# Performance work log

Hardware: AMD Instinct MI355X
Metric: run time of the kernel (lower is better)

The kernel has to match this reference:

```python
import jax, jax.numpy as jnp
import numpy as np

BIG = 3.4028234e+38  # torch fill value used as additive mask
EPS = 1e-5           # nn.LayerNorm default eps


def _layernorm(x):
    mu = jnp.mean(x, axis=-1, keepdims=True)
    var = jnp.mean(jnp.square(x - mu), axis=-1, keepdims=True)
    return (x - mu) / jnp.sqrt(var + EPS)


def setup_inputs() -> dict:
    key = jax.random.key(0)
    ks = jax.random.split(key, 12)
    B, N, H, S = 32, 512, 256, 3  # batch, num_codes, embedding_size, num_stacks
    features = jax.random.normal(ks[0], (B, N, H), dtype=jnp.float32)
    masks = jnp.ones((B, N, 1), dtype=jnp.float32)
    guide = jax.random.randint(ks[1], (B, N, N), 0, 2).astype(jnp.float32)
    prior_guide = jax.random.uniform(ks[2], (B, N, N), dtype=jnp.float32)
    sc = 0.02
    WQ = jax.random.normal(ks[3], (S, H, H), dtype=jnp.float32) * sc
    WK = jax.random.normal(ks[4], (S, H, H), dtype=jnp.float32) * sc
    WV = jax.random.normal(ks[5], (S, H, H), dtype=jnp.float32) * sc
    W1 = jax.random.normal(ks[6], (S, H, H), dtype=jnp.float32) * sc
    b1 = jnp.zeros((S, H), dtype=jnp.float32)
    W2 = jax.random.normal(ks[7], (S, H, H), dtype=jnp.float32) * sc
    b2 = jnp.zeros((S, H), dtype=jnp.float32)
    return {"features": features, "masks": masks, "guide": guide,
            "prior_guide": prior_guide, "WQ": WQ, "WK": WK, "WV": WV,
            "W1": W1, "b1": b1, "W2": W2, "b2": b2}


def reference(features, masks, guide, prior_guide, WQ, WK, WV, W1, b1, W2, b2):
    H = features.shape[-1]
    scale = 1.0 / jnp.sqrt(jnp.float32(H))
    attention_mask = jnp.where(masks[:, :, 0] != 0, 0.0, BIG)  # [B,N]
    inf_mask = jnp.where(guide != 0, 0.0, BIG)                 # [B,N,N]
    attentions = []
    x = features
    for i in range(WQ.shape[0]):
        f = masks * x                                          # [B,N,H]
        if i == 0:
            att = prior_guide[:, None, :, :]                   # use_prior path
        else:
            q = jnp.einsum('bnh,hd->bnd', f, WQ[i].T)          # nn.Linear: x @ W^T
            k = jnp.einsum('bnh,hd->bnd', f, WK[i].T)
            pre = jnp.einsum('bqd,bkd->bqk', q, k) * scale     # [B,N,N] (heads=1)
            pre = pre - attention_mask[:, None, :] - inf_mask
            att = jax.nn.softmax(pre, axis=-1)[:, None, :, :]  # [B,1,N,N]
        attentions.append(att)
        v = jnp.einsum('bnh,hd->bnd', f, WV[i].T)              # [B,N,H]
        post = jnp.einsum('bqk,bkh->bqh', att[:, 0], v)        # squeeze head dim
        post = _layernorm(post + f)
        ffn = jnp.maximum(jnp.einsum('bnh,hd->bnd', post, W1[i].T) + b1[i], 0.0)
        ffn = jnp.einsum('bnh,hd->bnd', ffn, W2[i].T) + b2[i]
        x = _layernorm(ffn + post)
    return x * masks, jnp.stack(attentions)
```

## Files before the change

kernel.cpp:

```cpp
#include <hip/hip_runtime.h>
#include <cstdint>
#include <cstddef>

#define B_ 32
#define N_ 512
#define H_ 256
#define S_ 3
#define BN_ (B_*N_)
#define HH_ (H_*H_)
#define BIGF 3.4028234e+38f
#define EPSF 1e-5f

typedef __bf16 bf16x8 __attribute__((ext_vector_type(8)));
typedef float  f32x4  __attribute__((ext_vector_type(4)));

typedef const void __attribute__((address_space(1)))* gas_t;
typedef void __attribute__((address_space(3)))* las_t;

__device__ __forceinline__ void async16(const unsigned short* g, unsigned short* l) {
  __builtin_amdgcn_global_load_lds((gas_t)g, (las_t)l, 16, 0, 0);
}

__device__ __forceinline__ unsigned short f2bf(float f) {
  __bf16 h = (__bf16)f;
  unsigned short s;
  __builtin_memcpy(&s, &h, 2);
  return s;
}
__device__ __forceinline__ float bf2f(unsigned short u) {
  unsigned int v = ((unsigned int)u) << 16;
  float f;
  __builtin_memcpy(&f, &v, 4);
  return f;
}

#define KC_STAGE(lane) ((((lane) & 3) ^ (((lane) >> 3) & 3)) * 8)
#define KC_READ(quad, l15) ((((quad) ^ (((l15) >> 1) & 3))) * 8)

__global__ __launch_bounds__(256) void cvt_all_k(
    const float* __restrict__ WQ, const float* __restrict__ WK,
    const float* __restrict__ WV, const float* __restrict__ W1,
    const float* __restrict__ W2,
    unsigned short* __restrict__ wqk, unsigned short* __restrict__ wv,
    unsigned short* __restrict__ w1, unsigned short* __restrict__ w2) {
  const int per = S_ * HH_ / 4;
  int gi = blockIdx.x * 256 + threadIdx.x;
  int which = gi / per;
  int e4 = gi - which * per;
  float4 v;
  if      (which == 0) v = ((const float4*)WQ)[e4];
  else if (which == 1) v = ((const float4*)WK)[e4];
  else if (which == 2) v = ((const float4*)WV)[e4];
  else if (which == 3) v = ((const float4*)W1)[e4];
  else                 v = ((const float4*)W2)[e4];
  ushort4 o;
  o.x = f2bf(v.x); o.y = f2bf(v.y); o.z = f2bf(v.z); o.w = f2bf(v.w);
  int e = e4 * 4;
  if (which <= 1) {
    int L = e / HH_, off = e - L * HH_;
    *(ushort4*)&wqk[(size_t)L * 2 * HH_ + (which == 1 ? HH_ : 0) + off] = o;
  } else if (which == 2) ((ushort4*)wv)[e4] = o;
  else if   (which == 3) ((ushort4*)w1)[e4] = o;
  else                   ((ushort4*)w2)[e4] = o;
}

__global__ __launch_bounds__(256) void mask_mul_k(
    const float* __restrict__ x, const float* __restrict__ masks,
    unsigned short* __restrict__ fb) {
  int i = blockIdx.x * 256 + threadIdx.x;
  int row = i >> 6;
  float m = masks[row];
  float4 v = ((const float4*)x)[i];
  ushort4 o;
  o.x = f2bf(v.x * m); o.y = f2bf(v.y * m); o.z = f2bf(v.z * m); o.w = f2bf(v.w * m);
  ((ushort4*)fb)[i] = o;
}

__global__ __launch_bounds__(256) void mfma_gemm_k(
    const unsigned short* __restrict__ A, const unsigned short* __restrict__ Bm,
    unsigned short* __restrict__ Cb,
    int K, int Nn, int lda, int ldb, long sA, long sB, long sC) {
  __shared__ __align__(16) unsigned short As[2][128 * 32];
  __shared__ __align__(16) unsigned short Bs[2][128 * 32];
  const int b = blockIdx.z;
  const int t = threadIdx.x;
  const int wave = t >> 6, lane = t & 63;
  const int wm = wave >> 1, wn = wave & 1;
  const int quad = lane >> 4, l15 = lane & 15;
  const int m0 = blockIdx.y * 128, n0 = blockIdx.x * 128;
  const int srow = lane >> 2;
  const int kc = KC_STAGE(lane);
  const int pos8 = (lane & 3) * 8;

  const unsigned short* pa0 = A + (size_t)b * sA + (size_t)(m0 + wave * 32 + srow) * lda + kc;
  const unsigned short* pa1 = pa0 + 16 * (size_t)lda;
  const unsigned short* pb0 = Bm + (size_t)b * sB + (size_t)(n0 + wave * 32 + srow) * ldb + kc;
  const unsigned short* pb1 = pb0 + 16 * (size_t)ldb;
  const int lo = (wave * 32 + srow) * 32 + pos8;

  f32x4 acc[4][4];
#pragma unroll
  for (int i = 0; i < 4; ++i)
#pragma unroll
    for (int j = 0; j < 4; ++j) acc[i][j] = (f32x4){0.f, 0.f, 0.f, 0.f};

  const int soff = KC_READ(quad, l15);
  const int NT = K >> 5;
  async16(pa0, &As[0][lo]); async16(pa1, &As[0][lo + 16 * 32]);
  async16(pb0, &Bs[0][lo]); async16(pb1, &Bs[0][lo + 16 * 32]);
  __syncthreads();
  int cur = 0;
  for (int tt = 0; tt < NT; ++tt) {
    if (tt + 1 < NT) {
      const int kn = (tt + 1) << 5;
      async16(pa0 + kn, &As[cur ^ 1][lo]); async16(pa1 + kn, &As[cur ^ 1][lo + 16 * 32]);
      async16(pb0 + kn, &Bs[cur ^ 1][lo]); async16(pb1 + kn, &Bs[cur ^ 1][lo + 16 * 32]);
    }
    bf16x8 af[4], bfr[4];
#pragma unroll
    for (int i = 0; i < 4; ++i)
      af[i] = *(const bf16x8*)&As[cur][(wm * 64 + i * 16 + l15) * 32 + soff];
#pragma unroll
    for (int j = 0; j < 4; ++j)
      bfr[j] = *(const bf16x8*)&Bs[cur][(wn * 64 + j * 16 + l15) * 32 + soff];
#pragma unroll
    for (int i = 0; i < 4; ++i)
#pragma unroll
      for (int j = 0; j < 4; ++j)
        acc[i][j] = __builtin_amdgcn_mfma_f32_16x16x32_bf16(af[i], bfr[j], acc[i][j], 0, 0, 0);
    __syncthreads();
    cur ^= 1;
  }

#pragma unroll
  for (int i = 0; i < 4; ++i) {
    const int rbase = m0 + wm * 64 + i * 16 + quad * 4;
#pragma unroll
    for (int j = 0; j < 4; ++j) {
      const int c = n0 + wn * 64 + j * 16 + l15;
#pragma unroll
      for (int r = 0; r < 4; ++r)
        Cb[(size_t)b * sC + (size_t)(rbase + r) * Nn + c] = f2bf(acc[i][j][r]);
    }
  }
}

template<int PRIOR>
__global__ __launch_bounds__(512) void ls_pv_k(
    const unsigned short* __restrict__ qk, const float* __restrict__ prior,
    const float* __restrict__ masks, const float* __restrict__ guide,
    const unsigned short* __restrict__ vT, const unsigned short* __restrict__ resb,
    float* __restrict__ att, float* __restrict__ post, unsigned short* __restrict__ postb) {
  __shared__ __align__(16) unsigned short As[2][64 * 32];
  __shared__ __align__(16) unsigned short Bs[2][512 * 32];
  __shared__ __align__(16) unsigned short Ps[64 * 520];
  __shared__ float red[4][64][2];
  const int b = blockIdx.x;
  const int t = threadIdx.x;
  const int wave = t >> 6, lane = t & 63;
  const int quad = lane >> 4, l15 = lane & 15;
  const int m0 = blockIdx.y * 64;
  const int srow = lane >> 2;
  const int kc = KC_STAGE(lane);
  const int pos8 = (lane & 3) * 8;
  const int soff = KC_READ(quad, l15);

  const unsigned short* vb = vT + (size_t)b * H_ * N_;
  const unsigned short* pv0 = vb + (size_t)(wave * 16 + srow) * N_ + kc;
  const unsigned short* pv1 = pv0 + (size_t)128 * N_;
  const int lvo = (wave * 16 + srow) * 32 + pos8;

  if (PRIOR) {
    async16(pv0, &Bs[0][lvo]);
    async16(pv1, &Bs[0][lvo + 128 * 32]);
    const float* src = prior + ((size_t)b * N_ + m0) * N_;
    float*       dst = att   + ((size_t)b * N_ + m0) * N_;
#pragma unroll
    for (int s = 0; s < 16; ++s) {
      int idx4 = s * 512 + t;
      float4 v = ((const float4*)src)[idx4];
      ((float4*)dst)[idx4] = v;
      int row = idx4 >> 7, col4 = idx4 & 127;
      ushort4 o;
      o.x = f2bf(v.x); o.y = f2bf(v.y); o.z = f2bf(v.z); o.w = f2bf(v.w);
      *(ushort4*)&Ps[row * 520 + col4 * 4] = o;
    }
    __syncthreads();
  } else {
    const int wm = wave >> 2, wn = wave & 3;
    const int ld = 2 * H_;
    const unsigned short* base = qk + (size_t)b * N_ * ld;
    const unsigned short* pa = base + (size_t)(m0 + wave * 16 + srow) * ld + kc;
    const unsigned short* pb = base + H_ + (size_t)(wave * 64 + srow) * ld + kc;
    const int lao = (wave * 16 + srow) * 32 + pos8;
    const int lbo = (wave * 64 + srow) * 32 + pos8;

    f32x4 acc[2][8];
#pragma unroll
    for (int i = 0; i < 2; ++i)
#pragma unroll
      for (int j = 0; j < 8; ++j) acc[i][j] = (f32x4){0.f, 0.f, 0.f, 0.f};

    if (wave < 4) async16(pa, &As[0][lao]);
#pragma unroll
    for (int c = 0; c < 4; ++c)
      async16(pb + (size_t)c * 16 * ld, &Bs[0][lbo + c * 16 * 32]);
    __syncthreads();
    int cur = 0;
#pragma unroll
    for (int tt = 0; tt < 8; ++tt) {
      if (tt < 7) {
        const int kn = (tt + 1) * 32;
        if (wave < 4) async16(pa + kn, &As[cur ^ 1][lao]);
#pragma unroll
        for (int c = 0; c < 4; ++c)
          async16(pb + (size_t)c * 16 * ld + kn, &Bs[cur ^ 1][lbo + c * 16 * 32]);
      }
      bf16x8 af[2], bfr[8];
#pragma unroll
      for (int i = 0; i < 2; ++i)
        af[i] = *(const bf16x8*)&As[cur][(wm * 32 + i * 16 + l15) * 32 + soff];
#pragma unroll
      for (int j = 0; j < 8; ++j)
        bfr[j] = *(const bf16x8*)&Bs[cur][(wn * 128 + j * 16 + l15) * 32 + soff];
#pragma unroll
      for (int i = 0; i < 2; ++i)
#pragma unroll
        for (int j = 0; j < 8; ++j)
          acc[i][j] = __builtin_amdgcn_mfma_f32_16x16x32_bf16(af[i], bfr[j], acc[i][j], 0, 0, 0);
      __syncthreads();
      cur ^= 1;
    }

    async16(pv0, &Bs[0][lvo]);
    async16(pv1, &Bs[0][lvo + 128 * 32]);

    float am[8];
#pragma unroll
    for (int j = 0; j < 8; ++j) {
      float mv = masks[(size_t)b * N_ + wn * 128 + j * 16 + l15];
      am[j] = (mv != 0.f) ? 0.f : BIGF;
    }
#pragma unroll
    for (int i = 0; i < 2; ++i) {
#pragma unroll
      for (int r = 0; r < 4; ++r) {
        const int mloc = wm * 32 + i * 16 + quad * 4 + r;
        const float* gr = guide + ((size_t)b * N_ + m0 + mloc) * N_;
        float mx = -BIGF;
#pragma unroll
        for (int j = 0; j < 8; ++j) {
          const int c = wn * 128 + j * 16 + l15;
          float g = gr[c];
          float v = acc[i][j][r] * 0.0625f - am[j] - ((g != 0.f) ? 0.f : BIGF);
          acc[i][j][r] = v;
          mx = fmaxf(mx, v);
        }
#pragma unroll
        for (int off = 1; off < 16; off <<= 1) mx = fmaxf(mx, __shfl_xor(mx, off));
        if (l15 == 0) red[wn][mloc][0] = mx;
      }
    }
    __syncthreads();
#pragma unroll
    for (int i = 0; i < 2; ++i) {
#pragma unroll
      for (int r = 0; r < 4; ++r) {
        const int mloc = wm * 32 + i * 16 + quad * 4 + r;
        float M = fmaxf(fmaxf(red[0][mloc][0], red[1][mloc][0]),
                        fmaxf(red[2][mloc][0], red[3][mloc][0]));
        float s = 0.f;
#pragma unroll
        for (int j = 0; j < 8; ++j) {
          float e = __expf(acc[i][j][r] - M);
          acc[i][j][r] = e;
          s += e;
        }
#pragma unroll
        for (int off = 1; off < 16; off <<= 1) s += __shfl_xor(s, off);
        if (l15 == 0) red[wn][mloc][1] = s;
      }
    }
    __syncthreads();
#pragma unroll
    for (int i = 0; i < 2; ++i) {
#pragma unroll
      for (int r = 0; r < 4; ++r) {
        const int mloc = wm * 32 + i * 16 + quad * 4 + r;
        float S = red[0][mloc][1] + red[1][mloc][1] + red[2][mloc][1] + red[3][mloc][1];
        float inv = 1.f / S;
        const size_t rowoff = ((size_t)b * N_ + m0 + mloc) * N_;
#pragma unroll
        for (int j = 0; j < 8; ++j) {
          const int c = wn * 128 + j * 16 + l15;
          float o = acc[i][j][r] * inv;
          att[rowoff + c] = o;
          Ps[mloc * 520 + c] = f2bf(o);
        }
      }
    }
    __syncthreads();
  }

  const int wm2 = wave >> 2, wn2 = wave & 3;

  f32x4 acc2[2][4];
#pragma unroll
  for (int i = 0; i < 2; ++i)
#pragma unroll
    for (int j = 0; j < 4; ++j) acc2[i][j] = (f32x4){0.f, 0.f, 0.f, 0.f};

  int cur = 0;
#pragma unroll
  for (int tt = 0; tt < 16; ++tt) {
    if (tt < 15) {
      const int kn = (tt + 1) * 32;
      async16(pv0 + kn, &Bs[cur ^ 1][lvo]);
      async16(pv1 + kn, &Bs[cur ^ 1][lvo + 128 * 32]);
    }
    bf16x8 af[2], bfr[4];
#pragma unroll
    for (int i = 0; i < 2; ++i)
      af[i] = *(const bf16x8*)&Ps[(wm2 * 32 + i * 16 + l15) * 520 + tt * 32 + quad * 8];
#pragma unroll
    for (int j = 0; j < 4; ++j)
      bfr[j] = *(const bf16x8*)&Bs[cur][(wn2 * 64 + j * 16 + l15) * 32 + soff];
#pragma unroll
    for (int i = 0; i < 2; ++i)
#pragma unroll
      for (int j = 0; j < 4; ++j)
        acc2[i][j] = __builtin_amdgcn_mfma_f32_16x16x32_bf16(af[i], bfr[j], acc2[i][j], 0, 0, 0);
    __syncthreads();
    cur ^= 1;
  }

#pragma unroll
  for (int i = 0; i < 2; ++i) {
#pragma unroll
    for (int r = 0; r < 4; ++r) {
      const int mloc = wm2 * 32 + i * 16 + quad * 4 + r;
      const long grow = (long)b * N_ + m0 + mloc;
      float s = 0.f, q = 0.f;
#pragma unroll
      for (int j = 0; j < 4; ++j) {
        const int c = wn2 * 64 + j * 16 + l15;
        float v = acc2[i][j][r] + bf2f(resb[grow * H_ + c]);
        acc2[i][j][r] = v;
        s += v; q += v * v;
      }
#pragma unroll
      for (int off = 1; off < 16; off <<= 1) {
        s += __shfl_xor(s, off);
        q += __shfl_xor(q, off);
      }
      if (l15 == 0) { red[wn2][mloc][0] = s; red[wn2][mloc][1] = q; }
    }
  }
  __syncthreads();
#pragma unroll
  for (int i = 0; i < 2; ++i) {
#pragma unroll
    for (int r = 0; r < 4; ++r) {
      const int mloc = wm2 * 32 + i * 16 + quad * 4 + r;
      const long grow = (long)b * N_ + m0 + mloc;
      float S = red[0][mloc][0] + red[1][mloc][0] + red[2][mloc][0] + red[3][mloc][0];
      float Q = red[0][mloc][1] + red[1][mloc][1] + red[2][mloc][1] + red[3][mloc][1];
      float mu = S * (1.f / H_);
      float var = Q * (1.f / H_) - mu * mu;
      float inv = 1.f / sqrtf(var + EPSF);
#pragma unroll
      for (int j = 0; j < 4; ++j) {
        const int c = wn2 * 64 + j * 16 + l15;
        float o = (acc2[i][j][r] - mu) * inv;
        post[grow * H_ + c] = o;
        postb[grow * H_ + c] = f2bf(o);
      }
    }
  }
}

template<int LAST>
__global__ __launch_bounds__(512) void ffn_k(
    const unsigned short* __restrict__ postb, const float* __restrict__ postf,
    const unsigned short* __restrict__ w1, const float* __restrict__ b1,
    const unsigned short* __restrict__ w2, const float* __restrict__ b2,
    const float* __restrict__ masks,
    unsigned short* __restrict__ fb, float* __restrict__ outx) {
  __shared__ __align__(16) unsigned short As[2][64 * 32];
  __shared__ __align__(16) unsigned short Bs[2][256 * 32];
  __shared__ __align__(16) unsigned short T1[64 * 264];
  __shared__ float red[4][64][2];
  const int t = threadIdx.x;
  const int wave = t >> 6, lane = t & 63;
  const int wm = wave >> 2, wn = wave & 3;
  const int quad = lane >> 4, l15 = lane & 15;
  const int m0 = blockIdx.y * 64;
  const int srow = lane >> 2;
  const int kc = KC_STAGE(lane);
  const int pos8 = (lane & 3) * 8;
  const int soff = KC_READ(quad, l15);

  const unsigned short* pa = postb + (size_t)(m0 + wave * 16 + srow) * H_ + kc;
  const int lao = (wave * 16 + srow) * 32 + pos8;
  const int lbo = (wave * 16 + srow) * 32 + pos8;

  const unsigned short* qb0 = w2 + (size_t)(wave * 16 + srow) * H_ + kc;
  const unsigned short* qb1 = qb0 + (size_t)128 * H_;

  {
    const unsigned short* pb0 = w1 + (size_t)(wave * 16 + srow) * H_ + kc;
    const unsigned short* pb1 = pb0 + (size_t)128 * H_;
    f32x4 acc[2][4];
#pragma unroll
    for (int i = 0; i < 2; ++i)
#pragma unroll
      for (int j = 0; j < 4; ++j) acc[i][j] = (f32x4){0.f, 0.f, 0.f, 0.f};
    if (wave < 4) async16(pa, &As[0][lao]);
    async16(pb0, &Bs[0][lbo]);
    async16(pb1, &Bs[0][lbo + 128 * 32]);
    __syncthreads();
    int cur = 0;
#pragma unroll
    for (int tt = 0; tt < 8; ++tt) {
      if (tt < 7) {
        const int kn = (tt + 1) * 32;
        if (wave < 4) async16(pa + kn, &As[cur ^ 1][lao]);
        async16(pb0 + kn, &Bs[cur ^ 1][lbo]);
        async16(pb1 + kn, &Bs[cur ^ 1][lbo + 128 * 32]);
      }
      bf16x8 af[2], bfr[4];
#pragma unroll
      for (int i = 0; i < 2; ++i)
        af[i] = *(const bf16x8*)&As[cur][(wm * 32 + i * 16 + l15) * 32 + soff];
#pragma unroll
      for (int j = 0; j < 4; ++j)
        bfr[j] = *(const bf16x8*)&Bs[cur][(wn * 64 + j * 16 + l15) * 32 + soff];
#pragma unroll
      for (int i = 0; i < 2; ++i)
#pragma unroll
        for (int j = 0; j < 4; ++j)
          acc[i][j] = __builtin_amdgcn_mfma_f32_16x16x32_bf16(af[i], bfr[j], acc[i][j], 0, 0, 0);
      __syncthreads();
      cur ^= 1;
    }

    async16(qb0, &Bs[0][lbo]);
    async16(qb1, &Bs[0][lbo + 128 * 32]);

    float bv[4];
#pragma unroll
    for (int j = 0; j < 4; ++j) bv[j] = b1[wn * 64 + j * 16 + l15];
#pragma unroll
    for (int i = 0; i < 2; ++i) {
#pragma unroll
      for (int r = 0; r < 4; ++r) {
        const int mloc = wm * 32 + i * 16 + quad * 4 + r;
#pragma unroll
        for (int j = 0; j < 4; ++j) {
          const int c = wn * 64 + j * 16 + l15;
          T1[mloc * 264 + c] = f2bf(fmaxf(acc[i][j][r] + bv[j], 0.f));
        }
      }
    }
  }
  __syncthreads();

  {
    f32x4 acc[2][4];
#pragma unroll
    for (int i = 0; i < 2; ++i)
#pragma unroll
      for (int j = 0; j < 4; ++j) acc[i][j] = (f32x4){0.f, 0.f, 0.f, 0.f};
    int cur = 0;
#pragma unroll
    for (int tt = 0; tt < 8; ++tt) {
      if (tt < 7) {
        const int kn = (tt + 1) * 32;
        async16(qb0 + kn, &Bs[cur ^ 1][lbo]);
        async16(qb1 + kn, &Bs[cur ^ 1][lbo + 128 * 32]);
      }
      bf16x8 af[2], bfr[4];
#pragma unroll
      for (int i = 0; i < 2; ++i)
        af[i] = *(const bf16x8*)&T1[(wm * 32 + i * 16 + l15) * 264 + tt * 32 + quad * 8];
#pragma unroll
      for (int j = 0; j < 4; ++j)
        bfr[j] = *(const bf16x8*)&Bs[cur][(wn * 64 + j * 16 + l15) * 32 + soff];
#pragma unroll
      for (int i = 0; i < 2; ++i)
#pragma unroll
        for (int j = 0; j < 4; ++j)
          acc[i][j] = __builtin_amdgcn_mfma_f32_16x16x32_bf16(af[i], bfr[j], acc[i][j], 0, 0, 0);
      __syncthreads();
      cur ^= 1;
    }
    float bv[4];
#pragma unroll
    for (int j = 0; j < 4; ++j) bv[j] = b2[wn * 64 + j * 16 + l15];
#pragma unroll
    for (int i = 0; i < 2; ++i) {
#pragma unroll
      for (int r = 0; r < 4; ++r) {
        const int mloc = wm * 32 + i * 16 + quad * 4 + r;
        const long grow = (long)m0 + mloc;
        float s = 0.f, q = 0.f;
#pragma unroll
        for (int j = 0; j < 4; ++j) {
          const int c = wn * 64 + j * 16 + l15;
          float v = acc[i][j][r] + bv[j] + postf[grow * H_ + c];
          acc[i][j][r] = v;
          s += v; q += v * v;
        }
#pragma unroll
        for (int off = 1; off < 16; off <<= 1) {
          s += __shfl_xor(s, off);
          q += __shfl_xor(q, off);
        }
        if (l15 == 0) { red[wn][mloc][0] = s; red[wn][mloc][1] = q; }
      }
    }
    __syncthreads();
#pragma unroll
    for (int i = 0; i < 2; ++i) {
#pragma unroll
      for (int r = 0; r < 4; ++r) {
        const int mloc = wm * 32 + i * 16 + quad * 4 + r;
        const long grow = (long)m0 + mloc;
        float S = red[0][mloc][0] + red[1][mloc][0] + red[2][mloc][0] + red[3][mloc][0];
        float Q = red[0][mloc][1] + red[1][mloc][1] + red[2][mloc][1] + red[3][mloc][1];
        float mu = S * (1.f / H_);
        float var = Q * (1.f / H_) - mu * mu;
        float inv = 1.f / sqrtf(var + EPSF);
        float mval = masks[grow];
#pragma unroll
        for (int j = 0; j < 4; ++j) {
          const int c = wn * 64 + j * 16 + l15;
          float o = (acc[i][j][r] - mu) * inv * mval;
          if (LAST) outx[grow * H_ + c] = o;
          else      fb[grow * H_ + c] = f2bf(o);
        }
      }
    }
  }
}

extern "C" void kernel_launch(void* const* d_in, const int* in_sizes, int n_in,
                              void* d_out, int out_size, void* d_ws, size_t ws_size,
                              hipStream_t stream) {
  const float* features = (const float*)d_in[0];
  const float* masks    = (const float*)d_in[1];
  const float* guide    = (const float*)d_in[2];
  const float* prior    = (const float*)d_in[3];
  const float* WQ       = (const float*)d_in[4];
  const float* WK       = (const float*)d_in[5];
  const float* WV       = (const float*)d_in[6];
  const float* W1       = (const float*)d_in[7];
  const float* b1       = (const float*)d_in[8];
  const float* W2       = (const float*)d_in[9];
  const float* b2       = (const float*)d_in[10];

  float* out     = (float*)d_out;
  float* out_x   = out;
  float* out_att = out + (size_t)BN_ * H_;

  char* w = (char*)d_ws;
  float* post = (float*)w;                     w += (size_t)BN_ * H_ * 4;
  unsigned short* f_bf   = (unsigned short*)w; w += (size_t)BN_ * H_ * 2;
  unsigned short* qk_bf  = (unsigned short*)w; w += (size_t)BN_ * 2 * H_ * 2;
  unsigned short* post_bf= (unsigned short*)w; w += (size_t)BN_ * H_ * 2;
  unsigned short* vT     = (unsigned short*)w; w += (size_t)BN_ * H_ * 2;
  unsigned short* wqk_bf = (unsigned short*)w; w += (size_t)S_ * 2 * HH_ * 2;
  unsigned short* wv_bf  = (unsigned short*)w; w += (size_t)S_ * HH_ * 2;
  unsigned short* w1_bf  = (unsigned short*)w; w += (size_t)S_ * HH_ * 2;
  unsigned short* w2_bf  = (unsigned short*)w; w += (size_t)S_ * HH_ * 2;

  dim3 g_cvt(5 * S_ * HH_ / 1024);
  dim3 g_ew(BN_ * H_ / 1024);
  dim3 g_qkp(4, BN_ / 128, 1);
  dim3 g_vt(4, 2, B_);
  dim3 g_ls(B_, N_ / 64, 1);
  dim3 g_ffn(1, BN_ / 64, 1);

  cvt_all_k<<<g_cvt, 256, 0, stream>>>(WQ, WK, WV, W1, W2, wqk_bf, wv_bf, w1_bf, w2_bf);
  mask_mul_k<<<g_ew, 256, 0, stream>>>(features, masks, f_bf);

  const long sF  = (long)N_ * H_;
  const long sVT = (long)H_ * N_;

  for (int i = 0; i < S_; ++i) {
    float* att = out_att + (size_t)i * B_ * N_ * N_;
    mfma_gemm_k<<<g_vt, 256, 0, stream>>>(wv_bf + (size_t)i * HH_, f_bf, vT,
                                          H_, N_, H_, H_, 0, sF, sVT);
    if (i == 0) {
      ls_pv_k<1><<<g_ls, 512, 0, stream>>>(nullptr, prior, nullptr, nullptr,
                                           vT, f_bf, att, post, post_bf);
    } else {
      mfma_gemm_k<<<g_qkp, 256, 0, stream>>>(f_bf, wqk_bf + (size_t)i * 2 * HH_, qk_bf,
                                             H_, 2 * H_, H_, H_, 0, 0, 0);
      ls_pv_k<0><<<g_ls, 512, 0, stream>>>(qk_bf, nullptr, masks, guide,
                                           vT, f_bf, att, post, post_bf);
    }
    if (i < S_ - 1) {
      ffn_k<0><<<g_ffn, 512, 0, stream>>>(post_bf, post,
          w1_bf + (size_t)i * HH_, b1 + (size_t)i * H_,
          w2_bf + (size_t)i * HH_, b2 + (size_t)i * H_, masks, f_bf, nullptr);
    } else {
      ffn_k<1><<<g_ffn, 512, 0, stream>>>(post_bf, post,
          w1_bf + (size_t)i * HH_, b1 + (size_t)i * H_,
          w2_bf + (size_t)i * HH_, b2 + (size_t)i * H_, masks, nullptr, out_x);
    }
  }
}
```

Before: 377.8 us.

## Fuse FFN into attention kernel and merge QK and V projection launches

The attention/PV/LayerNorm kernel now continues straight into the two FFN GEMMs and the final LayerNorm. The post-attention tile stays in registers and shared memory instead of being written to global memory as fp32 and bf16 and read back by a separate FFN kernel. The QK and V projection GEMMs for stacks after the first are combined into a single launch using a flattened block index. This removes a global-memory round trip and several launches, at the cost of a larger shared-memory footprint, more register pressure in one long kernel, and an in-place overwrite of f_bf.

```diff
diff --git a/kernel.cpp b/kernel.cpp
--- a/kernel.cpp
+++ b/kernel.cpp
@@ -10,6 +10,8 @@
 #define HH_ (H_*H_)
 #define BIGF 3.4028234e+38f
 #define EPSF 1e-5f
+#define SF_ ((long)N_ * H_)
+#define SVT_ ((long)H_ * N_)
 
 typedef __bf16 bf16x8 __attribute__((ext_vector_type(8)));
 typedef float  f32x4  __attribute__((ext_vector_type(4)));
@@ -76,18 +78,15 @@
   ((ushort4*)fb)[i] = o;
 }
 
-__global__ __launch_bounds__(256) void mfma_gemm_k(
+__device__ __forceinline__ void gemm_body(
     const unsigned short* __restrict__ A, const unsigned short* __restrict__ Bm,
     unsigned short* __restrict__ Cb,
-    int K, int Nn, int lda, int ldb, long sA, long sB, long sC) {
-  __shared__ __align__(16) unsigned short As[2][128 * 32];
-  __shared__ __align__(16) unsigned short Bs[2][128 * 32];
-  const int b = blockIdx.z;
-  const int t = threadIdx.x;
+    int K, int Nn, int lda, int ldb, long sA, long sB, long sC,
+    int b, int m0, int n0, int t,
+    unsigned short (&As)[2][128 * 32], unsigned short (&Bs)[2][128 * 32]) {
   const int wave = t >> 6, lane = t & 63;
   const int wm = wave >> 1, wn = wave & 1;
   const int quad = lane >> 4, l15 = lane & 15;
-  const int m0 = blockIdx.y * 128, n0 = blockIdx.x * 128;
   const int srow = lane >> 2;
   const int kc = KC_STAGE(lane);
   const int pos8 = (lane & 3) * 8;
@@ -145,15 +144,46 @@
   }
 }
 
-template<int PRIOR>
-__global__ __launch_bounds__(512) void ls_pv_k(
+__global__ __launch_bounds__(256) void mfma_gemm_k(
+    const unsigned short* __restrict__ A, const unsigned short* __restrict__ Bm,
+    unsigned short* __restrict__ Cb,
+    int K, int Nn, int lda, int ldb, long sA, long sB, long sC) {
+  __shared__ __align__(16) unsigned short As[2][128 * 32];
+  __shared__ __align__(16) unsigned short Bs[2][128 * 32];
+  gemm_body(A, Bm, Cb, K, Nn, lda, ldb, sA, sB, sC,
+            blockIdx.z, blockIdx.y * 128, blockIdx.x * 128, threadIdx.x, As, Bs);
+}
+
+__global__ __launch_bounds__(256) void gemm2_k(
+    const unsigned short* __restrict__ A1, const unsigned short* __restrict__ B1,
+    unsigned short* __restrict__ C1,
+    const unsigned short* __restrict__ A2, const unsigned short* __restrict__ B2,
+    unsigned short* __restrict__ C2) {
+  __shared__ __align__(16) unsigned short As[2][128 * 32];
+  __shared__ __align__(16) unsigned short Bs[2][128 * 32];
+  const int bx = blockIdx.x;
+  if (bx < 512) {
+    gemm_body(A1, B1, C1, H_, 2 * H_, H_, H_, 0, 0, 0,
+              0, (bx >> 2) * 128, (bx & 3) * 128, threadIdx.x, As, Bs);
+  } else {
+    const int v = bx - 512;
+    gemm_body(A2, B2, C2, H_, N_, H_, H_, 0, SF_, SVT_,
+              v >> 3, ((v >> 2) & 1) * 128, (v & 3) * 128, threadIdx.x, As, Bs);
+  }
+}
+
+template<int PRIOR, int LAST>
+__global__ __launch_bounds__(512) void mega_k(
     const unsigned short* __restrict__ qk, const float* __restrict__ prior,
     const float* __restrict__ masks, const float* __restrict__ guide,
     const unsigned short* __restrict__ vT, const unsigned short* __restrict__ resb,
-    float* __restrict__ att, float* __restrict__ post, unsigned short* __restrict__ postb) {
+    const unsigned short* __restrict__ w1, const float* __restrict__ b1,
+    const unsigned short* __restrict__ w2, const float* __restrict__ b2,
+    float* __restrict__ att, unsigned short* __restrict__ fbout,
+    float* __restrict__ outx) {
   __shared__ __align__(16) unsigned short As[2][64 * 32];
   __shared__ __align__(16) unsigned short Bs[2][512 * 32];
-  __shared__ __align__(16) unsigned short Ps[64 * 520];
+  __shared__ __align__(16) unsigned short PsU[64 * 528];
   __shared__ float red[4][64][2];
   const int b = blockIdx.x;
   const int t = threadIdx.x;
@@ -165,7 +195,7 @@
   const int pos8 = (lane & 3) * 8;
   const int soff = KC_READ(quad, l15);
 
-  const unsigned short* vb = vT + (size_t)b * H_ * N_;
+  const unsigned short* vb = vT + (size_t)b * SVT_;
   const unsigned short* pv0 = vb + (size_t)(wave * 16 + srow) * N_ + kc;
   const unsigned short* pv1 = pv0 + (size_t)128 * N_;
   const int lvo = (wave * 16 + srow) * 32 + pos8;
@@ -183,7 +213,7 @@
       int row = idx4 >> 7, col4 = idx4 & 127;
       ushort4 o;
       o.x = f2bf(v.x); o.y = f2bf(v.y); o.z = f2bf(v.z); o.w = f2bf(v.w);
-      *(ushort4*)&Ps[row * 520 + col4 * 4] = o;
+      *(ushort4*)&PsU[row * 520 + col4 * 4] = o;
     }
     __syncthreads();
   } else {
@@ -295,7 +325,7 @@
           const int c = wn * 128 + j * 16 + l15;
           float o = acc[i][j][r] * inv;
           att[rowoff + c] = o;
-          Ps[mloc * 520 + c] = f2bf(o);
+          PsU[mloc * 520 + c] = f2bf(o);
         }
       }
     }
@@ -321,7 +351,7 @@
     bf16x8 af[2], bfr[4];
 #pragma unroll
     for (int i = 0; i < 2; ++i)
-      af[i] = *(const bf16x8*)&Ps[(wm2 * 32 + i * 16 + l15) * 520 + tt * 32 + quad * 8];
+      af[i] = *(const bf16x8*)&PsU[(wm2 * 32 + i * 16 + l15) * 520 + tt * 32 + quad * 8];
 #pragma unroll
     for (int j = 0; j < 4; ++j)
       bfr[j] = *(const bf16x8*)&Bs[cur][(wn2 * 64 + j * 16 + l15) * 32 + soff];
@@ -333,6 +363,13 @@
     __syncthreads();
     cur ^= 1;
   }
+
+  const unsigned short* pw1  = w1 + (size_t)(wave * 16 + srow) * H_ + kc;
+  const unsigned short* pw1b = pw1 + (size_t)128 * H_;
+  const unsigned short* pw2  = w2 + (size_t)(wave * 16 + srow) * H_ + kc;
+  const unsigned short* pw2b = pw2 + (size_t)128 * H_;
+  async16(pw1,  &Bs[0][lvo]);
+  async16(pw1b, &Bs[0][lvo + 128 * 32]);
 
 #pragma unroll
   for (int i = 0; i < 2; ++i) {
@@ -357,12 +394,13 @@
     }
   }
   __syncthreads();
+  unsigned short* Pb  = PsU;
+  unsigned short* T1p = PsU + 64 * 264;
 #pragma unroll
   for (int i = 0; i < 2; ++i) {
 #pragma unroll
     for (int r = 0; r < 4; ++r) {
       const int mloc = wm2 * 32 + i * 16 + quad * 4 + r;
-      const long grow = (long)b * N_ + m0 + mloc;
       float S = red[0][mloc][0] + red[1][mloc][0] + red[2][mloc][0] + red[3][mloc][0];
       float Q = red[0][mloc][1] + red[1][mloc][1] + red[2][mloc][1] + red[3][mloc][1];
       float mu = S * (1.f / H_);
@@ -372,93 +410,58 @@
       for (int j = 0; j < 4; ++j) {
         const int c = wn2 * 64 + j * 16 + l15;
         float o = (acc2[i][j][r] - mu) * inv;
-        post[grow * H_ + c] = o;
-        postb[grow * H_ + c] = f2bf(o);
-      }
-    }
-  }
-}
-
-template<int LAST>
-__global__ __launch_bounds__(512) void ffn_k(
-    const unsigned short* __restrict__ postb, const float* __restrict__ postf,
-    const unsigned short* __restrict__ w1, const float* __restrict__ b1,
-    const unsigned short* __restrict__ w2, const float* __restrict__ b2,
-    const float* __restrict__ masks,
-    unsigned short* __restrict__ fb, float* __restrict__ outx) {
-  __shared__ __align__(16) unsigned short As[2][64 * 32];
-  __shared__ __align__(16) unsigned short Bs[2][256 * 32];
-  __shared__ __align__(16) unsigned short T1[64 * 264];
-  __shared__ float red[4][64][2];
-  const int t = threadIdx.x;
-  const int wave = t >> 6, lane = t & 63;
-  const int wm = wave >> 2, wn = wave & 3;
-  const int quad = lane >> 4, l15 = lane & 15;
-  const int m0 = blockIdx.y * 64;
-  const int srow = lane >> 2;
-  const int kc = KC_STAGE(lane);
-  const int pos8 = (lane & 3) * 8;
-  const int soff = KC_READ(quad, l15);
-
-  const unsigned short* pa = postb + (size_t)(m0 + wave * 16 + srow) * H_ + kc;
-  const int lao = (wave * 16 + srow) * 32 + pos8;
-  const int lbo = (wave * 16 + srow) * 32 + pos8;
-
-  const unsigned short* qb0 = w2 + (size_t)(wave * 16 + srow) * H_ + kc;
-  const unsigned short* qb1 = qb0 + (size_t)128 * H_;
+        acc2[i][j][r] = o;
+        Pb[mloc * 264 + c] = f2bf(o);
+      }
+    }
+  }
+  __syncthreads();
 
   {
-    const unsigned short* pb0 = w1 + (size_t)(wave * 16 + srow) * H_ + kc;
-    const unsigned short* pb1 = pb0 + (size_t)128 * H_;
-    f32x4 acc[2][4];
+    f32x4 acc3[2][4];
 #pragma unroll
     for (int i = 0; i < 2; ++i)
 #pragma unroll
-      for (int j = 0; j < 4; ++j) acc[i][j] = (f32x4){0.f, 0.f, 0.f, 0.f};
-    if (wave < 4) async16(pa, &As[0][lao]);
-    async16(pb0, &Bs[0][lbo]);
-    async16(pb1, &Bs[0][lbo + 128 * 32]);
-    __syncthreads();
-    int cur = 0;
+      for (int j = 0; j < 4; ++j) acc3[i][j] = (f32x4){0.f, 0.f, 0.f, 0.f};
+    cur = 0;
 #pragma unroll
     for (int tt = 0; tt < 8; ++tt) {
       if (tt < 7) {
         const int kn = (tt + 1) * 32;
-        if (wave < 4) async16(pa + kn, &As[cur ^ 1][lao]);
-        async16(pb0 + kn, &Bs[cur ^ 1][lbo]);
-        async16(pb1 + kn, &Bs[cur ^ 1][lbo + 128 * 32]);
+        async16(pw1  + kn, &Bs[cur ^ 1][lvo]);
+        async16(pw1b + kn, &Bs[cur ^ 1][lvo + 128 * 32]);
       }
       bf16x8 af[2], bfr[4];
 #pragma unroll
       for (int i = 0; i < 2; ++i)
-        af[i] = *(const bf16x8*)&As[cur][(wm * 32 + i * 16 + l15) * 32 + soff];
+        af[i] = *(const bf16x8*)&Pb[(wm2 * 32 + i * 16 + l15) * 264 + tt * 32 + quad * 8];
 #pragma unroll
       for (int j = 0; j < 4; ++j)
-        bfr[j] = *(const bf16x8*)&Bs[cur][(wn * 64 + j * 16 + l15) * 32 + soff];
+        bfr[j] = *(const bf16x8*)&Bs[cur][(wn2 * 64 + j * 16 + l15) * 32 + soff];
 #pragma unroll
       for (int i = 0; i < 2; ++i)
 #pragma unroll
         for (int j = 0; j < 4; ++j)
-          acc[i][j] = __builtin_amdgcn_mfma_f32_16x16x32_bf16(af[i], bfr[j], acc[i][j], 0, 0, 0);
+          acc3[i][j] = __builtin_amdgcn_mfma_f32_16x16x32_bf16(af[i], bfr[j], acc3[i][j], 0, 0, 0);
       __syncthreads();
       cur ^= 1;
     }
 
-    async16(qb0, &Bs[0][lbo]);
-    async16(qb1, &Bs[0][lbo + 128 * 32]);
+    async16(pw2,  &Bs[0][lvo]);
+    async16(pw2b, &Bs[0][lvo + 128 * 32]);
 
     float bv[4];
 #pragma unroll
-    for (int j = 0; j < 4; ++j) bv[j] = b1[wn * 64 + j * 16 + l15];
+    for (int j = 0; j < 4; ++j) bv[j] = b1[wn2 * 64 + j * 16 + l15];
 #pragma unroll
     for (int i = 0; i < 2; ++i) {
 #pragma unroll
       for (int r = 0; r < 4; ++r) {
-        const int mloc = wm * 32 + i * 16 + quad * 4 + r;
+        const int mloc = wm2 * 32 + i * 16 + quad * 4 + r;
 #pragma unroll
         for (int j = 0; j < 4; ++j) {
-          const int c = wn * 64 + j * 16 + l15;
-          T1[mloc * 264 + c] = f2bf(fmaxf(acc[i][j][r] + bv[j], 0.f));
+          const int c = wn2 * 64 + j * 16 + l15;
+          T1p[mloc * 264 + c] = f2bf(fmaxf(acc3[i][j][r] + bv[j], 0.f));
         }
       }
     }
@@ -466,49 +469,47 @@
   __syncthreads();
 
   {
-    f32x4 acc[2][4];
+    f32x4 acc4[2][4];
 #pragma unroll
     for (int i = 0; i < 2; ++i)
 #pragma unroll
-      for (int j = 0; j < 4; ++j) acc[i][j] = (f32x4){0.f, 0.f, 0.f, 0.f};
-    int cur = 0;
+      for (int j = 0; j < 4; ++j) acc4[i][j] = (f32x4){0.f, 0.f, 0.f, 0.f};
+    cur = 0;
 #pragma unroll
     for (int tt = 0; tt < 8; ++tt) {
       if (tt < 7) {
         const int kn = (tt + 1) * 32;
-        async16(qb0 + kn, &Bs[cur ^ 1][lbo]);
-        async16(qb1 + kn, &Bs[cur ^ 1][lbo + 128 * 32]);
+        async16(pw2  + kn, &Bs[cur ^ 1][lvo]);
+        async16(pw2b + kn, &Bs[cur ^ 1][lvo + 128 * 32]);
       }
       bf16x8 af[2], bfr[4];
 #pragma unroll
       for (int i = 0; i < 2; ++i)
-        af[i] = *(const bf16x8*)&T1[(wm * 32 + i * 16 + l15) * 264 + tt * 32 + quad * 8];
+        af[i] = *(const bf16x8*)&T1p[(wm2 * 32 + i * 16 + l15) * 264 + tt * 32 + quad * 8];
 #pragma unroll
       for (int j = 0; j < 4; ++j)
-        bfr[j] = *(const bf16x8*)&Bs[cur][(wn * 64 + j * 16 + l15) * 32 + soff];
+        bfr[j] = *(const bf16x8*)&Bs[cur][(wn2 * 64 + j * 16 + l15) * 32 + soff];
 #pragma unroll
       for (int i = 0; i < 2; ++i)
 #pragma unroll
         for (int j = 0; j < 4; ++j)
-          acc[i][j] = __builtin_amdgcn_mfma_f32_16x16x32_bf16(af[i], bfr[j], acc[i][j], 0, 0, 0);
+          acc4[i][j] = __builtin_amdgcn_mfma_f32_16x16x32_bf16(af[i], bfr[j], acc4[i][j], 0, 0, 0);
       __syncthreads();
       cur ^= 1;
     }
     float bv[4];
 #pragma unroll
-    for (int j = 0; j < 4; ++j) bv[j] = b2[wn * 64 + j * 16 + l15];
+    for (int j = 0; j < 4; ++j) bv[j] = b2[wn2 * 64 + j * 16 + l15];
 #pragma unroll
     for (int i = 0; i < 2; ++i) {
 #pragma unroll
       for (int r = 0; r < 4; ++r) {
-        const int mloc = wm * 32 + i * 16 + quad * 4 + r;
-        const long grow = (long)m0 + mloc;
+        const int mloc = wm2 * 32 + i * 16 + quad * 4 + r;
         float s = 0.f, q = 0.f;
 #pragma unroll
         for (int j = 0; j < 4; ++j) {
-          const int c = wn * 64 + j * 16 + l15;
-          float v = acc[i][j][r] + bv[j] + postf[grow * H_ + c];
-          acc[i][j][r] = v;
+          float v = acc4[i][j][r] + bv[j] + acc2[i][j][r];
+          acc4[i][j][r] = v;
           s += v; q += v * v;
         }
 #pragma unroll
@@ -516,7 +517,7 @@
           s += __shfl_xor(s, off);
           q += __shfl_xor(q, off);
         }
-        if (l15 == 0) { red[wn][mloc][0] = s; red[wn][mloc][1] = q; }
+        if (l15 == 0) { red[wn2][mloc][0] = s; red[wn2][mloc][1] = q; }
       }
     }
     __syncthreads();
@@ -524,8 +525,8 @@
     for (int i = 0; i < 2; ++i) {
 #pragma unroll
       for (int r = 0; r < 4; ++r) {
-        const int mloc = wm * 32 + i * 16 + quad * 4 + r;
-        const long grow = (long)m0 + mloc;
+        const int mloc = wm2 * 32 + i * 16 + quad * 4 + r;
+        const long grow = (long)b * N_ + m0 + mloc;
         float S = red[0][mloc][0] + red[1][mloc][0] + red[2][mloc][0] + red[3][mloc][0];
         float Q = red[0][mloc][1] + red[1][mloc][1] + red[2][mloc][1] + red[3][mloc][1];
         float mu = S * (1.f / H_);
@@ -534,10 +535,10 @@
         float mval = masks[grow];
 #pragma unroll
         for (int j = 0; j < 4; ++j) {
-          const int c = wn * 64 + j * 16 + l15;
-          float o = (acc[i][j][r] - mu) * inv * mval;
+          const int c = wn2 * 64 + j * 16 + l15;
+          float o = (acc4[i][j][r] - mu) * inv * mval;
           if (LAST) outx[grow * H_ + c] = o;
-          else      fb[grow * H_ + c] = f2bf(o);
+          else      fbout[grow * H_ + c] = f2bf(o);
         }
       }
     }
@@ -564,10 +565,8 @@
   float* out_att = out + (size_t)BN_ * H_;
 
   char* w = (char*)d_ws;
-  float* post = (float*)w;                     w += (size_t)BN_ * H_ * 4;
   unsigned short* f_bf   = (unsigned short*)w; w += (size_t)BN_ * H_ * 2;
   unsigned short* qk_bf  = (unsigned short*)w; w += (size_t)BN_ * 2 * H_ * 2;
-  unsigned short* post_bf= (unsigned short*)w; w += (size_t)BN_ * H_ * 2;
   unsigned short* vT     = (unsigned short*)w; w += (size_t)BN_ * H_ * 2;
   unsigned short* wqk_bf = (unsigned short*)w; w += (size_t)S_ * 2 * HH_ * 2;
   unsigned short* wv_bf  = (unsigned short*)w; w += (size_t)S_ * HH_ * 2;
@@ -576,38 +575,36 @@
 
   dim3 g_cvt(5 * S_ * HH_ / 1024);
   dim3 g_ew(BN_ * H_ / 1024);
-  dim3 g_qkp(4, BN_ / 128, 1);
   dim3 g_vt(4, 2, B_);
-  dim3 g_ls(B_, N_ / 64, 1);
-  dim3 g_ffn(1, BN_ / 64, 1);
+  dim3 g_g2(768);
+  dim3 g_mega(B_, N_ / 64);
 
   cvt_all_k<<<g_cvt, 256, 0, stream>>>(WQ, WK, WV, W1, W2, wqk_bf, wv_bf, w1_bf, w2_bf);
   mask_mul_k<<<g_ew, 256, 0, stream>>>(features, masks, f_bf);
 
-  const long sF  = (long)N_ * H_;
-  const long sVT = (long)H_ * N_;
-
   for (int i = 0; i < S_; ++i) {
     float* att = out_att + (size_t)i * B_ * N_ * N_;
-    mfma_gemm_k<<<g_vt, 256, 0, stream>>>(wv_bf + (size_t)i * HH_, f_bf, vT,
-                                          H_, N_, H_, H_, 0, sF, sVT);
+    const unsigned short* w1p = w1_bf + (size_t)i * HH_;
+    const unsigned short* w2p = w2_bf + (size_t)i * HH_;
+    const float* b1p = b1 + (size_t)i * H_;
+    const float* b2p = b2 + (size_t)i * H_;
     if (i == 0) {
-      ls_pv_k<1><<<g_ls, 512, 0, stream>>>(nullptr, prior, nullptr, nullptr,
-                                           vT, f_bf, att, post, post_bf);
+      mfma_gemm_k<<<g_vt, 256, 0, stream>>>(wv_bf, f_bf, vT, H_, N_, H_, H_, 0, SF_, SVT_);
+      mega_k<1, 0><<<g_mega, 512, 0, stream>>>(nullptr, prior, masks, nullptr,
+                                               vT, f_bf, w1p, b1p, w2p, b2p,
+                                               att, f_bf, nullptr);
     } else {
-      mfma_gemm_k<<<g_qkp, 256, 0, stream>>>(f_bf, wqk_bf + (size_t)i * 2 * HH_, qk_bf,
-                                             H_, 2 * H_, H_, H_, 0, 0, 0);
-      ls_pv_k<0><<<g_ls, 512, 0, stream>>>(qk_bf, nullptr, masks, guide,
-                                           vT, f_bf, att, post, post_bf);
-    }
-    if (i < S_ - 1) {
-      ffn_k<0><<<g_ffn, 512, 0, stream>>>(post_bf, post,
-          w1_bf + (size_t)i * HH_, b1 + (size_t)i * H_,
-          w2_bf + (size_t)i * HH_, b2 + (size_t)i * H_, masks, f_bf, nullptr);
-    } else {
-      ffn_k<1><<<g_ffn, 512, 0, stream>>>(post_bf, post,
-          w1_bf + (size_t)i * HH_, b1 + (size_t)i * H_,
-          w2_bf + (size_t)i * HH_, b2 + (size_t)i * H_, masks, nullptr, out_x);
-    }
-  }
-}
+      gemm2_k<<<g_g2, 256, 0, stream>>>(f_bf, wqk_bf + (size_t)i * 2 * HH_, qk_bf,
+                                        wv_bf + (size_t)i * HH_, f_bf, vT);
+      if (i < S_ - 1) {
+        mega_k<0, 0><<<g_mega, 512, 0, stream>>>(qk_bf, nullptr, masks, guide,
+                                                 vT, f_bf, w1p, b1p, w2p, b2p,
+                                                 att, f_bf, nullptr);
+      } else {
+        mega_k<0, 1><<<g_mega, 512, 0, stream>>>(qk_bf, nullptr, masks, guide,
+                                                 vT, f_bf, w1p, b1p, w2p, b2p,
+                                                 att, nullptr, out_x);
+      }
+    }
+  }
+}
```

Result: faster. 339.3 us (-10.2%).
